# Kernel optimization log

Measured on AMD Instinct MI355X. Metric: run time of the kernel, lower is better.

## Reference

```python
import jax, jax.numpy as jnp
import numpy as np

N, D, E, L, H, F1, G, A = 4096, 256, 131072, 3, 4, 128, 16, 32

def setup_inputs() -> dict:
    key = jax.random.key(0)
    ks = jax.random.split(key, 12)
    s = lambda k, shape, fan: jax.random.normal(k, shape, jnp.float32) / np.sqrt(fan)
    return {
        "x": jax.random.normal(ks[0], (N, D), jnp.float32),
        "edge_attr": jax.random.uniform(ks[1], (E,), jnp.float32),
        "conv_Wself": s(ks[2], (L, D, D), D),
        "conv_Wnbr": s(ks[3], (L, D, D), D),
        "conv_b": jnp.zeros((L, D), jnp.float32),
        "bn_gamma": jnp.ones((L - 1, D), jnp.float32),
        "bn_beta": jnp.zeros((L - 1, D), jnp.float32),
        "bn_mean": jnp.zeros((L - 1, D), jnp.float32),
        "bn_var": jnp.ones((L - 1, D), jnp.float32),
        "Wqkv": s(ks[4], (3, D, D), D),
        "bqkv": jnp.zeros((3, D), jnp.float32),
        "Wo": s(ks[5], (D, D), D),
        "bo": jnp.zeros((D,), jnp.float32),
        "fc1_W": s(ks[6], (D, F1), D),
        "fc1_b": jnp.zeros((F1,), jnp.float32),
        "AW1": s(ks[7], (G, F1, A), F1),
        "Ab1": jnp.zeros((G, A), jnp.float32),
        "AW2": s(ks[8], (G, A, 1), A),
        "Ab2": jnp.zeros((G, 1), jnp.float32),
        "edge_index": jax.random.randint(ks[9], (2, E), 0, N, jnp.int32),
        "node_groups": jax.random.randint(ks[10], (N,), 0, G, jnp.int32),
    }


def reference(x, edge_attr, conv_Wself, conv_Wnbr, conv_b, bn_gamma, bn_beta,
              bn_mean, bn_var, Wqkv, bqkv, Wo, bo, fc1_W, fc1_b,
              AW1, Ab1, AW2, Ab2, edge_index, node_groups):
    src, dst = edge_index[0], edge_index[1]
    # message-passing conv stack (edge_attr only used by the last, non-attention layer)
    for i in range(L):
        msg = x[src]
        if i == L - 1:
            msg = msg * edge_attr[:, None]
        agg = jax.ops.segment_sum(msg, dst, num_segments=N)
        x = x @ conv_Wself[i] + agg @ conv_Wnbr[i] + conv_b[i]
        if i < L - 1:
            x = bn_gamma[i] * (x - bn_mean[i]) * jax.lax.rsqrt(bn_var[i] + 1e-5) + bn_beta[i]
            x = jax.nn.elu(x)
    # hierarchy self-attention over all N nodes (batch of 1), residual add
    dh = D // H
    q = (x @ Wqkv[0] + bqkv[0]).reshape(N, H, dh)
    k = (x @ Wqkv[1] + bqkv[1]).reshape(N, H, dh)
    v = (x @ Wqkv[2] + bqkv[2]).reshape(N, H, dh)
    scores = jnp.einsum('nhd,mhd->hnm', q, k) / np.sqrt(dh).astype(np.float32)
    attn = jax.nn.softmax(scores, axis=-1)
    o = jnp.einsum('hnm,mhd->nhd', attn, v).reshape(N, D) @ Wo + bo
    x = x + o
    feats = jax.nn.elu(x @ fc1_W + fc1_b)  # [N, F1]; dropout is eval no-op
    # MoE-style per-node group adapter routing: gather tiny MLP weights per node
    h = jax.nn.relu(jnp.einsum('nd,nda->na', feats, AW1[node_groups]) + Ab1[node_groups])
    out = jnp.einsum('na,nao->no', h, AW2[node_groups]) + Ab2[node_groups]  # [N, 1]
    return out
```

## Files before the change

### kernel.cpp

```cpp
#include <hip/hip_runtime.h>
#include <math.h>

#define NN   4096
#define DIM  256
#define NE   131072
#define NH   4
#define DH   64
#define F1D  128
#define NG   16
#define AD   32

typedef unsigned short u16;
typedef unsigned int   u32;
typedef _Float16 f16;
typedef __attribute__((ext_vector_type(8))) _Float16 half8;
typedef __attribute__((ext_vector_type(4))) float f32x4;

enum { EPI_BIAS = 0, EPI_BNELU = 1 };
enum { MEPI_WO = 0, MEPI_FC1 = 1 };

#define MFMA16(a, b, c) __builtin_amdgcn_mfma_f32_16x16x32_f16(a, b, c, 0, 0, 0)

__device__ inline u16 f2h(float x) { union { f16 f; u16 u; } c; c.f = (f16)x; return c.u; }
__device__ inline void split16(float x, u16& h, u16& l) {
    union { f16 f; u16 u; } ch, cl;
    ch.f = (f16)x;
    cl.f = (f16)(x - (float)ch.f);
    h = ch.u; l = cl.u;
}

__global__ void csr_count(const int* __restrict__ dst, int* __restrict__ cnt) {
    int e = blockIdx.x * 256 + threadIdx.x;
    atomicAdd(&cnt[dst[e]], 1);
}

__global__ __launch_bounds__(1024) void csr_scan(
    int* __restrict__ cnt, int* __restrict__ off)
{
    __shared__ int wsum[16];
    const int t = threadIdx.x;
    const int lane = t & 63;
    int4 v = *(const int4*)&cnt[t * 4];
    const int s = v.x + v.y + v.z + v.w;
    int acc = s;
    #pragma unroll
    for (int o = 1; o < 64; o <<= 1) {
        int u = __shfl_up(acc, o);
        if (lane >= o) acc += u;
    }
    if (lane == 63) wsum[t >> 6] = acc;
    __syncthreads();
    if (t < 16) {
        int w0 = wsum[t];
        int a2 = w0;
        #pragma unroll
        for (int o = 1; o < 16; o <<= 1) {
            int u = __shfl_up(a2, o);
            if (t >= o) a2 += u;
        }
        wsum[t] = a2 - w0;
    }
    __syncthreads();
    const int base = wsum[t >> 6] + (acc - s);
    off[t * 4 + 0] = base;
    off[t * 4 + 1] = base + v.x;
    off[t * 4 + 2] = base + v.x + v.y;
    off[t * 4 + 3] = base + v.x + v.y + v.z;
    *(int4*)&cnt[t * 4] = make_int4(0, 0, 0, 0);
    if (t == 1023) off[NN] = base + s;
}

__global__ void csr_fill(const int* __restrict__ dst, const int* __restrict__ src,
                         const float* __restrict__ eattr, const int* __restrict__ off,
                         int* __restrict__ cur, int* __restrict__ esrc,
                         float* __restrict__ ewt) {
    int e = blockIdx.x * 256 + threadIdx.x;
    int d = dst[e];
    int pos = off[d] + atomicAdd(&cur[d], 1);
    esrc[pos] = src[e];
    ewt[pos]  = eattr[e];
}

__global__ __launch_bounds__(256) void prep_kernel(
    const float* __restrict__ x,
    const float* __restrict__ Ws, const float* __restrict__ Wn,
    const float* __restrict__ Wqkv, const float* __restrict__ Wo,
    const float* __restrict__ fc1W,
    u16* __restrict__ xh, u16* __restrict__ xl,
    u16* __restrict__ wch, u16* __restrict__ wcl,
    u16* __restrict__ w4h, u16* __restrict__ w4l,
    u16* __restrict__ f1h, u16* __restrict__ f1l,
    int* __restrict__ cur)
{
    const int b = blockIdx.x;
    const int t = threadIdx.x;
    if (b < 1024) {
        const int gid = b * 256 + t;
        const float4 v = *(const float4*)&x[(size_t)gid * 4];
        u16 h[4], l[4];
        split16(v.x, h[0], l[0]); split16(v.y, h[1], l[1]);
        split16(v.z, h[2], l[2]); split16(v.w, h[3], l[3]);
        *(uint2*)&xh[(size_t)gid * 4] =
            make_uint2((u32)h[0] | ((u32)h[1] << 16), (u32)h[2] | ((u32)h[3] << 16));
        *(uint2*)&xl[(size_t)gid * 4] =
            make_uint2((u32)l[0] | ((u32)l[1] << 16), (u32)l[2] | ((u32)l[3] << 16));
    } else if (b < 1408) {
        const int gid = (b - 1024) * 256 + t;
        const int L = gid / 32768;
        const int rem = gid % 32768;
        const int m = rem / 128;
        const int k4 = (rem % 128) * 4;
        const float* S = Ws + (size_t)L * 65536;
        const float* Nb = Wn + (size_t)L * 65536;
        u16 h[4], l[4];
        #pragma unroll
        for (int j = 0; j < 4; ++j) {
            const int k = k4 + j;
            const float v = (k < 256) ? S[(size_t)k * 256 + m]
                                      : Nb[(size_t)(k - 256) * 256 + m];
            split16(v, h[j], l[j]);
        }
        const size_t o = (size_t)L * 131072 + (size_t)m * 512 + k4;
        *(uint2*)&wch[o] = make_uint2((u32)h[0] | ((u32)h[1] << 16), (u32)h[2] | ((u32)h[3] << 16));
        *(uint2*)&wcl[o] = make_uint2((u32)l[0] | ((u32)l[1] << 16), (u32)l[2] | ((u32)l[3] << 16));
    } else if (b < 1664) {
        const int gid = (b - 1408) * 256 + t;
        const int mat = gid / 16384;
        const int rem = gid % 16384;
        const int m = rem / 64;
        const int k4 = (rem % 64) * 4;
        const float* W = (mat < 3) ? Wqkv + (size_t)mat * 65536 : Wo;
        u16 h[4], l[4];
        #pragma unroll
        for (int j = 0; j < 4; ++j)
            split16(W[(size_t)(k4 + j) * 256 + m], h[j], l[j]);
        const size_t o = (size_t)mat * 65536 + (size_t)m * 256 + k4;
        *(uint2*)&w4h[o] = make_uint2((u32)h[0] | ((u32)h[1] << 16), (u32)h[2] | ((u32)h[3] << 16));
        *(uint2*)&w4l[o] = make_uint2((u32)l[0] | ((u32)l[1] << 16), (u32)l[2] | ((u32)l[3] << 16));
    } else if (b < 1696) {
        const int gid = (b - 1664) * 256 + t;
        const int m = gid / 64;
        const int k4 = (gid % 64) * 4;
        u16 h[4], l[4];
        #pragma unroll
        for (int j = 0; j < 4; ++j)
            split16(fc1W[(size_t)(k4 + j) * F1D + m], h[j], l[j]);
        const size_t o = (size_t)m * 256 + k4;
        *(uint2*)&f1h[o] = make_uint2((u32)h[0] | ((u32)h[1] << 16), (u32)h[2] | ((u32)h[3] << 16));
        *(uint2*)&f1l[o] = make_uint2((u32)l[0] | ((u32)l[1] << 16), (u32)l[2] | ((u32)l[3] << 16));
    } else {
        const int gid = (b - 1696) * 256 + t;
        if (gid < NN / 4) *(int4*)&cur[gid * 4] = make_int4(0, 0, 0, 0);
    }
}

template<bool LAST>
__global__ __launch_bounds__(256) void agg_kernel(
    const float* __restrict__ x, const int* __restrict__ esrc,
    const float* __restrict__ ewt, const int* __restrict__ off,
    u16* __restrict__ aggh, u16* __restrict__ aggl)
{
    const int node = blockIdx.x * 4 + (threadIdx.x >> 6);
    const int lane = threadIdx.x & 63;
    const int d4 = lane * 4;
    int j = off[node];
    const int j1 = off[node + 1];
    float4 acc = make_float4(0.f, 0.f, 0.f, 0.f);
    for (; j + 4 <= j1; j += 4) {
        const int s0 = esrc[j], s1 = esrc[j + 1], s2 = esrc[j + 2], s3 = esrc[j + 3];
        const float4 x0 = *(const float4*)&x[(size_t)s0 * DIM + d4];
        const float4 x1 = *(const float4*)&x[(size_t)s1 * DIM + d4];
        const float4 x2 = *(const float4*)&x[(size_t)s2 * DIM + d4];
        const float4 x3 = *(const float4*)&x[(size_t)s3 * DIM + d4];
        const float w0 = LAST ? ewt[j]     : 1.f;
        const float w1 = LAST ? ewt[j + 1] : 1.f;
        const float w2 = LAST ? ewt[j + 2] : 1.f;
        const float w3 = LAST ? ewt[j + 3] : 1.f;
        acc.x = fmaf(x0.x, w0, acc.x); acc.y = fmaf(x0.y, w0, acc.y);
        acc.z = fmaf(x0.z, w0, acc.z); acc.w = fmaf(x0.w, w0, acc.w);
        acc.x = fmaf(x1.x, w1, acc.x); acc.y = fmaf(x1.y, w1, acc.y);
        acc.z = fmaf(x1.z, w1, acc.z); acc.w = fmaf(x1.w, w1, acc.w);
        acc.x = fmaf(x2.x, w2, acc.x); acc.y = fmaf(x2.y, w2, acc.y);
        acc.z = fmaf(x2.z, w2, acc.z); acc.w = fmaf(x2.w, w2, acc.w);
        acc.x = fmaf(x3.x, w3, acc.x); acc.y = fmaf(x3.y, w3, acc.y);
        acc.z = fmaf(x3.z, w3, acc.z); acc.w = fmaf(x3.w, w3, acc.w);
    }
    for (; j < j1; ++j) {
        const int s = esrc[j];
        const float w = LAST ? ewt[j] : 1.f;
        const float4 xv = *(const float4*)&x[(size_t)s * DIM + d4];
        acc.x = fmaf(xv.x, w, acc.x); acc.y = fmaf(xv.y, w, acc.y);
        acc.z = fmaf(xv.z, w, acc.z); acc.w = fmaf(xv.w, w, acc.w);
    }
    u16 h[4], l[4];
    split16(acc.x, h[0], l[0]); split16(acc.y, h[1], l[1]);
    split16(acc.z, h[2], l[2]); split16(acc.w, h[3], l[3]);
    *(uint2*)&aggh[(size_t)node * DIM + d4] =
        make_uint2((u32)h[0] | ((u32)h[1] << 16), (u32)h[2] | ((u32)h[3] << 16));
    *(uint2*)&aggl[(size_t)node * DIM + d4] =
        make_uint2((u32)l[0] | ((u32)l[1] << 16), (u32)l[2] | ((u32)l[3] << 16));
}

template<int EPI>
__global__ __launch_bounds__(256) void conv_mfma(
    const u16* __restrict__ xh, const u16* __restrict__ xl,
    const u16* __restrict__ gh, const u16* __restrict__ gl,
    const u16* __restrict__ bth, const u16* __restrict__ btl,
    const float* __restrict__ bias,
    const float* __restrict__ gamma, const float* __restrict__ beta,
    const float* __restrict__ bnmean, const float* __restrict__ bnvar,
    float* __restrict__ outf, u16* __restrict__ oh, u16* __restrict__ ol)
{
    __shared__ u16 lds[13824];
    u16* As_h = lds;
    u16* As_l = lds + 2304;
    u16* Bs_h = lds + 4608;
    u16* Bs_l = lds + 9216;
    #define TKP 72

    const int tid  = threadIdx.x;
    const int row0 = blockIdx.y * 32;
    const int col0 = blockIdx.x * 64;

    const int w   = tid >> 6;
    const int l15 = tid & 15, h4 = (tid & 63) >> 4;
    const int rh  = w & 1, ch = w >> 1;
    const int arow = tid >> 3, acs = (tid & 7) * 8;
    const int brow = tid & 63, bseg = tid >> 6;
    const int bc = bseg * 16;

    uint4 sah, sal, sbh0, sbh1, sbl0, sbl1;
    {
        sah = *((const uint4*)&xh[(size_t)(row0 + arow) * DIM + acs]);
        sal = *((const uint4*)&xl[(size_t)(row0 + arow) * DIM + acs]);
        const u16* pbh = bth + (size_t)(col0 + brow) * 512 + bc;
        const u16* pbl = btl + (size_t)(col0 + brow) * 512 + bc;
        sbh0 = ((const uint4*)pbh)[0]; sbh1 = ((const uint4*)pbh)[1];
        sbl0 = ((const uint4*)pbl)[0]; sbl1 = ((const uint4*)pbl)[1];
    }

    const f32x4 z4 = {0.f, 0.f, 0.f, 0.f};
    f32x4 acc[2] = {z4, z4};

    for (int kt = 0; kt < 8; ++kt) {
        *(uint4*)&As_h[arow * TKP + acs] = sah;
        *(uint4*)&As_l[arow * TKP + acs] = sal;
        *(uint4*)&Bs_h[brow * TKP + bc]     = sbh0;
        *(uint4*)&Bs_h[brow * TKP + bc + 8] = sbh1;
        *(uint4*)&Bs_l[brow * TKP + bc]     = sbl0;
        *(uint4*)&Bs_l[brow * TKP + bc + 8] = sbl1;
        if (kt + 1 < 8) {
            const int kn = kt + 1;
            const u16 *pah, *pal;
            if (kn < 4) {
                pah = xh + (size_t)(row0 + arow) * DIM + kn * 64 + acs;
                pal = xl + (size_t)(row0 + arow) * DIM + kn * 64 + acs;
            } else {
                pah = gh + (size_t)(row0 + arow) * DIM + (kn - 4) * 64 + acs;
                pal = gl + (size_t)(row0 + arow) * DIM + (kn - 4) * 64 + acs;
            }
            sah = *((const uint4*)pah);
            sal = *((const uint4*)pal);
            const u16* pbh = bth + (size_t)(col0 + brow) * 512 + kn * 64 + bc;
            const u16* pbl = btl + (size_t)(col0 + brow) * 512 + kn * 64 + bc;
            sbh0 = ((const uint4*)pbh)[0]; sbh1 = ((const uint4*)pbh)[1];
            sbl0 = ((const uint4*)pbl)[0]; sbl1 = ((const uint4*)pbl)[1];
        }
        __syncthreads();

        __builtin_amdgcn_s_setprio(1);
        #pragma unroll
        for (int kc = 0; kc < 2; ++kc) {
            const int dc = kc * 32 + h4 * 8;
            half8 afh, afl, bfh[2], bfl[2];
            afh = *(const half8*)&As_h[(rh * 16 + l15) * TKP + dc];
            afl = *(const half8*)&As_l[(rh * 16 + l15) * TKP + dc];
            #pragma unroll
            for (int bb = 0; bb < 2; ++bb) {
                const int r = ch * 32 + bb * 16 + l15;
                bfh[bb] = *(const half8*)&Bs_h[r * TKP + dc];
                bfl[bb] = *(const half8*)&Bs_l[r * TKP + dc];
            }
            #pragma unroll
            for (int bb = 0; bb < 2; ++bb) {
                acc[bb] = MFMA16(afh, bfh[bb], acc[bb]);
                acc[bb] = MFMA16(afh, bfl[bb], acc[bb]);
                acc[bb] = MFMA16(afl, bfh[bb], acc[bb]);
            }
        }
        __builtin_amdgcn_s_setprio(0);
        __syncthreads();
    }

    #pragma unroll
    for (int bb = 0; bb < 2; ++bb) {
        const int c  = col0 + ch * 32 + bb * 16 + l15;
        const int r0 = row0 + rh * 16 + h4 * 4;
        #pragma unroll
        for (int i = 0; i < 4; ++i) {
            const int r = r0 + i;
            float t = acc[bb][i] + bias[c];
            if (EPI == EPI_BNELU) {
                t = gamma[c] * (t - bnmean[c]) * rsqrtf(bnvar[c] + 1e-5f) + beta[c];
                t = t > 0.f ? t : expm1f(t);
            }
            outf[(size_t)r * DIM + c] = t;
            u16 hh, ll;
            split16(t, hh, ll);
            oh[(size_t)r * DIM + c] = hh;
            ol[(size_t)r * DIM + c] = ll;
        }
    }
    #undef TKP
}

__global__ __launch_bounds__(256) void qkv_mfma(
    const u16* __restrict__ xh, const u16* __restrict__ xl,
    const u16* __restrict__ wth, const u16* __restrict__ wtl,
    const float* __restrict__ bias,
    u16* __restrict__ qh_o, u16* __restrict__ ql_o,
    u16* __restrict__ kh_o, u16* __restrict__ kl_o,
    u16* __restrict__ vt_o)
{
    __shared__ u16 lds[4 * 4608];
    u16* As_h = lds;
    u16* As_l = lds + 4608;
    u16* Bs_h = lds + 9216;
    u16* Bs_l = lds + 13824;
    #define TKP 72

    const int tid  = threadIdx.x;
    const int row0 = blockIdx.y * 64;
    const int mat  = blockIdx.x >> 2;
    const int col0 = (blockIdx.x & 3) * 64;
    const float* biasp = bias + mat * DIM;

    const int w   = tid >> 6;
    const int l15 = tid & 15, h4 = (tid & 63) >> 4;
    const int rh  = w & 1, ch = w >> 1;
    const int lrow = tid & 63, lseg = tid >> 6;
    const int lc = lseg * 16;

    const size_t brow = (size_t)(mat * 256 + col0 + lrow) * 256;
    uint4 sah0, sah1, sal0, sal1, sbh0, sbh1, sbl0, sbl1;
    {
        const u16* pah = xh + (size_t)(row0 + lrow) * DIM + lc;
        const u16* pal = xl + (size_t)(row0 + lrow) * DIM + lc;
        sah0 = ((const uint4*)pah)[0]; sah1 = ((const uint4*)pah)[1];
        sal0 = ((const uint4*)pal)[0]; sal1 = ((const uint4*)pal)[1];
        sbh0 = ((const uint4*)(wth + brow + lc))[0]; sbh1 = ((const uint4*)(wth + brow + lc))[1];
        sbl0 = ((const uint4*)(wtl + brow + lc))[0]; sbl1 = ((const uint4*)(wtl + brow + lc))[1];
    }

    const f32x4 z4 = {0.f, 0.f, 0.f, 0.f};
    f32x4 acc[2][2] = {{z4, z4}, {z4, z4}};

    for (int kt = 0; kt < 4; ++kt) {
        *(uint4*)&As_h[lrow * TKP + lc]     = sah0;
        *(uint4*)&As_h[lrow * TKP + lc + 8] = sah1;
        *(uint4*)&As_l[lrow * TKP + lc]     = sal0;
        *(uint4*)&As_l[lrow * TKP + lc + 8] = sal1;
        *(uint4*)&Bs_h[lrow * TKP + lc]     = sbh0;
        *(uint4*)&Bs_h[lrow * TKP + lc + 8] = sbh1;
        *(uint4*)&Bs_l[lrow * TKP + lc]     = sbl0;
        *(uint4*)&Bs_l[lrow * TKP + lc + 8] = sbl1;
        if (kt + 1 < 4) {
            const int kb = (kt + 1) * 64 + lc;
            const u16* pah = xh + (size_t)(row0 + lrow) * DIM + kb;
            const u16* pal = xl + (size_t)(row0 + lrow) * DIM + kb;
            sah0 = ((const uint4*)pah)[0]; sah1 = ((const uint4*)pah)[1];
            sal0 = ((const uint4*)pal)[0]; sal1 = ((const uint4*)pal)[1];
            sbh0 = ((const uint4*)(wth + brow + kb))[0]; sbh1 = ((const uint4*)(wth + brow + kb))[1];
            sbl0 = ((const uint4*)(wtl + brow + kb))[0]; sbl1 = ((const uint4*)(wtl + brow + kb))[1];
        }
        __syncthreads();

        __builtin_amdgcn_s_setprio(1);
        #pragma unroll
        for (int kc = 0; kc < 2; ++kc) {
            const int dc = kc * 32 + h4 * 8;
            half8 afh[2], afl[2], bfh[2], bfl[2];
            #pragma unroll
            for (int ab = 0; ab < 2; ++ab) {
                const int r = rh * 32 + ab * 16 + l15;
                afh[ab] = *(const half8*)&As_h[r * TKP + dc];
                afl[ab] = *(const half8*)&As_l[r * TKP + dc];
            }
            #pragma unroll
            for (int bb = 0; bb < 2; ++bb) {
                const int r = ch * 32 + bb * 16 + l15;
                bfh[bb] = *(const half8*)&Bs_h[r * TKP + dc];
                bfl[bb] = *(const half8*)&Bs_l[r * TKP + dc];
            }
            #pragma unroll
            for (int ab = 0; ab < 2; ++ab)
                #pragma unroll
                for (int bb = 0; bb < 2; ++bb) {
                    acc[ab][bb] = MFMA16(afh[ab], bfh[bb], acc[ab][bb]);
                    acc[ab][bb] = MFMA16(afh[ab], bfl[bb], acc[ab][bb]);
                    acc[ab][bb] = MFMA16(afl[ab], bfh[bb], acc[ab][bb]);
                }
        }
        __builtin_amdgcn_s_setprio(0);
        __syncthreads();
    }

    const float s = (mat == 0) ? 0.125f : 1.0f;
    u16* oph = (mat == 0) ? qh_o : kh_o;
    u16* opl = (mat == 0) ? ql_o : kl_o;
    #pragma unroll
    for (int ab = 0; ab < 2; ++ab)
        #pragma unroll
        for (int bb = 0; bb < 2; ++bb) {
            const int c  = col0 + ch * 32 + bb * 16 + l15;
            const int r0 = row0 + rh * 32 + ab * 16 + h4 * 4;
            if (mat < 2) {
                #pragma unroll
                for (int i = 0; i < 4; ++i) {
                    const int r = r0 + i;
                    const float t = (acc[ab][bb][i] + biasp[c]) * s;
                    u16 hh, ll;
                    split16(t, hh, ll);
                    oph[(size_t)r * DIM + c] = hh;
                    opl[(size_t)r * DIM + c] = ll;
                }
            } else {
                u16 v[4];
                #pragma unroll
                for (int i = 0; i < 4; ++i)
                    v[i] = f2h(acc[ab][bb][i] + biasp[c]);
                *(uint2*)&vt_o[(size_t)c * NN + r0] =
                    make_uint2((u32)v[0] | ((u32)v[1] << 16), (u32)v[2] | ((u32)v[3] << 16));
            }
        }
    #undef TKP
}

template<int MEPI>
__global__ __launch_bounds__(256) void mfma_gemm(
    const u16* __restrict__ Ah, const u16* __restrict__ Al,
    const u16* __restrict__ Bth, const u16* __restrict__ Btl,
    const float* __restrict__ bias, const float* __restrict__ resid,
    float* __restrict__ outf, u16* __restrict__ outh, u16* __restrict__ outl,
    int K, int M)
{
    __shared__ u16 lds[4 * 4608];
    u16* As_h = lds;
    u16* As_l = lds + 4608;
    u16* Bs_h = lds + 9216;
    u16* Bs_l = lds + 13824;
    #define TKP 72

    const int tid  = threadIdx.x;
    const int row0 = blockIdx.y * 64;
    const int col0 = blockIdx.x * 64;

    const int w   = tid >> 6;
    const int l15 = tid & 15, h4 = (tid & 63) >> 4;
    const int rh  = w & 1, ch = w >> 1;
    const int lrow = tid & 63, lseg = tid >> 6;
    const int lc = lseg * 16;

    uint4 sah0, sah1, sal0, sal1, sbh0, sbh1, sbl0, sbl1;
    {
        const u16* pa0 = Ah  + (size_t)(row0 + lrow) * K + lc;
        const u16* pa1 = Al  + (size_t)(row0 + lrow) * K + lc;
        const u16* pb0 = Bth + (size_t)(col0 + lrow) * K + lc;
        const u16* pb1 = Btl + (size_t)(col0 + lrow) * K + lc;
        sah0 = ((const uint4*)pa0)[0]; sah1 = ((const uint4*)pa0)[1];
        sal0 = ((const uint4*)pa1)[0]; sal1 = ((const uint4*)pa1)[1];
        sbh0 = ((const uint4*)pb0)[0]; sbh1 = ((const uint4*)pb0)[1];
        sbl0 = ((const uint4*)pb1)[0]; sbl1 = ((const uint4*)pb1)[1];
    }

    const f32x4 z4 = {0.f, 0.f, 0.f, 0.f};
    f32x4 acc[2][2] = {{z4, z4}, {z4, z4}};
    const int NKT2 = K / 64;

    for (int kt = 0; kt < NKT2; ++kt) {
        *(uint4*)&As_h[lrow * TKP + lc]     = sah0;
        *(uint4*)&As_h[lrow * TKP + lc + 8] = sah1;
        *(uint4*)&As_l[lrow * TKP + lc]     = sal0;
        *(uint4*)&As_l[lrow * TKP + lc + 8] = sal1;
        *(uint4*)&Bs_h[lrow * TKP + lc]     = sbh0;
        *(uint4*)&Bs_h[lrow * TKP + lc + 8] = sbh1;
        *(uint4*)&Bs_l[lrow * TKP + lc]     = sbl0;
        *(uint4*)&Bs_l[lrow * TKP + lc + 8] = sbl1;
        if (kt + 1 < NKT2) {
            const int kb = (kt + 1) * 64 + lc;
            const u16* pa0 = Ah  + (size_t)(row0 + lrow) * K + kb;
            const u16* pa1 = Al  + (size_t)(row0 + lrow) * K + kb;
            const u16* pb0 = Bth + (size_t)(col0 + lrow) * K + kb;
            const u16* pb1 = Btl + (size_t)(col0 + lrow) * K + kb;
            sah0 = ((const uint4*)pa0)[0]; sah1 = ((const uint4*)pa0)[1];
            sal0 = ((const uint4*)pa1)[0]; sal1 = ((const uint4*)pa1)[1];
            sbh0 = ((const uint4*)pb0)[0]; sbh1 = ((const uint4*)pb0)[1];
            sbl0 = ((const uint4*)pb1)[0]; sbl1 = ((const uint4*)pb1)[1];
        }
        __syncthreads();

        __builtin_amdgcn_s_setprio(1);
        #pragma unroll
        for (int kc = 0; kc < 2; ++kc) {
            const int dc = kc * 32 + h4 * 8;
            half8 afh[2], afl[2], bfh[2], bfl[2];
            #pragma unroll
            for (int ab = 0; ab < 2; ++ab) {
                const int r = rh * 32 + ab * 16 + l15;
                afh[ab] = *(const half8*)&As_h[r * TKP + dc];
                afl[ab] = *(const half8*)&As_l[r * TKP + dc];
            }
            #pragma unroll
            for (int bb = 0; bb < 2; ++bb) {
                const int r = ch * 32 + bb * 16 + l15;
                bfh[bb] = *(const half8*)&Bs_h[r * TKP + dc];
                bfl[bb] = *(const half8*)&Bs_l[r * TKP + dc];
            }
            #pragma unroll
            for (int ab = 0; ab < 2; ++ab)
                #pragma unroll
                for (int bb = 0; bb < 2; ++bb) {
                    acc[ab][bb] = MFMA16(afh[ab], bfh[bb], acc[ab][bb]);
                    acc[ab][bb] = MFMA16(afh[ab], bfl[bb], acc[ab][bb]);
                    acc[ab][bb] = MFMA16(afl[ab], bfh[bb], acc[ab][bb]);
                }
        }
        __builtin_amdgcn_s_setprio(0);
        __syncthreads();
    }

    #pragma unroll
    for (int ab = 0; ab < 2; ++ab)
        #pragma unroll
        for (int bb = 0; bb < 2; ++bb) {
            const int c  = col0 + ch * 32 + bb * 16 + l15;
            const int r0 = row0 + rh * 32 + ab * 16 + h4 * 4;
            #pragma unroll
            for (int i = 0; i < 4; ++i) {
                const int r = r0 + i;
                float t = acc[ab][bb][i] + bias[c];
                if (MEPI == MEPI_WO) {
                    t += resid[(size_t)r * M + c];
                    u16 hh, ll;
                    split16(t, hh, ll);
                    outh[(size_t)r * M + c] = hh;
                    outl[(size_t)r * M + c] = ll;
                } else {
                    t = t > 0.f ? t : expm1f(t);
                    outf[(size_t)r * M + c] = t;
                }
            }
        }
    #undef TKP
}

#define QB 64
#define KB 64
#define NSPLIT 4
#define NKT (NN / KB)
#define KP 72

__global__ __launch_bounds__(256, 2) void attn_kernel(
    const u16* __restrict__ qhi, const u16* __restrict__ qlo,
    const u16* __restrict__ khi, const u16* __restrict__ klo,
    const u16* __restrict__ vT,
    float* __restrict__ op0, float* __restrict__ op1,
    float* __restrict__ op2, float* __restrict__ op3,
    float* __restrict__ mpart, float* __restrict__ lpart)
{
    __shared__ u16 lds[32384];
    u16* Kh0 = lds;
    u16* Kl0 = lds + 4608;
    u16* Vt0 = lds + 9216;
    u16* Kh1 = lds + 13824;
    u16* Kl1 = lds + 18432;
    u16* Vt1 = lds + 23040;
    u16* Pb  = lds + 27648;
    u16* Qh  = lds;
    u16* Ql  = lds + 4608;
    float* frow = (float*)(lds + 32256);

    const int tid = threadIdx.x;
    const int h   = blockIdx.y;
    const int q0  = blockIdx.x * QB;
    const int sp  = blockIdx.z;
    const int kt0 = sp * (NKT / NSPLIT);
    const int kt1 = kt0 + NKT / NSPLIT;

    const int w   = tid >> 6;
    const int l15 = tid & 15, h4 = (tid & 63) >> 4;
    const int lrow = tid & 63, lseg = tid >> 6;
    const int gq = h * DH + lseg * 16;

    {
        const u16* s0 = qhi + (size_t)(q0 + lrow) * DIM + gq;
        const u16* s1 = qlo + (size_t)(q0 + lrow) * DIM + gq;
        uint4 a = ((const uint4*)s0)[0], b = ((const uint4*)s0)[1];
        uint4 c = ((const uint4*)s1)[0], d = ((const uint4*)s1)[1];
        *(uint4*)&Qh[lrow * KP + lseg * 16]     = a;
        *(uint4*)&Qh[lrow * KP + lseg * 16 + 8] = b;
        *(uint4*)&Ql[lrow * KP + lseg * 16]     = c;
        *(uint4*)&Ql[lrow * KP + lseg * 16 + 8] = d;
    }

    uint4 rk0, rk1, rl0, rl1, rv0, rv1;
    auto load_tile = [&](int kt_ld) {
        const int key0 = kt_ld * KB;
        const u16* s0 = khi + (size_t)(key0 + lrow) * DIM + gq;
        const u16* s1 = klo + (size_t)(key0 + lrow) * DIM + gq;
        const u16* s2 = vT + (size_t)(h * DH + lrow) * NN + key0 + lseg * 16;
        rk0 = ((const uint4*)s0)[0]; rk1 = ((const uint4*)s0)[1];
        rl0 = ((const uint4*)s1)[0]; rl1 = ((const uint4*)s1)[1];
        rv0 = ((const uint4*)s2)[0]; rv1 = ((const uint4*)s2)[1];
    };
    load_tile(kt0);
    __syncthreads();

    half8 qf[2][2];
    #pragma unroll
    for (int kc = 0; kc < 2; ++kc) {
        const int r = w * 16 + l15;
        const int dc = kc * 32 + h4 * 8;
        qf[kc][0] = *(const half8*)&Qh[r * KP + dc];
        qf[kc][1] = *(const half8*)&Ql[r * KP + dc];
    }
    __syncthreads();

    auto stage_to = [&](u16* Kh, u16* Kl, u16* Vt) {
        *(uint4*)&Kh[lrow * KP + lseg * 16]     = rk0;
        *(uint4*)&Kh[lrow * KP + lseg * 16 + 8] = rk1;
        *(uint4*)&Kl[lrow * KP + lseg * 16]     = rl0;
        *(uint4*)&Kl[lrow * KP + lseg * 16 + 8] = rl1;
        *(uint4*)&Vt[lrow * KP + lseg * 16]     = rv0;
        *(uint4*)&Vt[lrow * KP + lseg * 16 + 8] = rv1;
    };

    stage_to(Kh0, Kl0, Vt0);
    load_tile(kt0 + 1);
    __syncthreads();

    const f32x4 z4 = {0.f, 0.f, 0.f, 0.f};
    f32x4 oacc[4] = {z4, z4, z4, z4};
    float m_run[4], l_run[4];
    #pragma unroll
    for (int i = 0; i < 4; ++i) { m_run[i] = -3.0e38f; l_run[i] = 0.f; }

    auto tile_body = [&](int t, u16* Kc, u16* Lc, u16* Vc,
                         u16* Kn, u16* Ln, u16* Vn) {
        if (t + 1 < kt1) stage_to(Kn, Ln, Vn);
        if (t + 2 < kt1) load_tile(t + 2);

        f32x4 sc[4] = {z4, z4, z4, z4};
        __builtin_amdgcn_s_setprio(1);
        #pragma unroll
        for (int kc = 0; kc < 2; ++kc) {
            const int dc = kc * 32 + h4 * 8;
            half8 kfh[4], kfl[4];
            #pragma unroll
            for (int kcb = 0; kcb < 4; ++kcb) {
                const int r = kcb * 16 + l15;
                kfh[kcb] = *(const half8*)&Kc[r * KP + dc];
                kfl[kcb] = *(const half8*)&Lc[r * KP + dc];
            }
            #pragma unroll
            for (int kcb = 0; kcb < 4; ++kcb) {
                sc[kcb] = MFMA16(qf[kc][0], kfh[kcb], sc[kcb]);
                sc[kcb] = MFMA16(qf[kc][0], kfl[kcb], sc[kcb]);
                sc[kcb] = MFMA16(qf[kc][1], kfh[kcb], sc[kcb]);
            }
        }
        __builtin_amdgcn_s_setprio(0);
        float p[4][4], fr[4];
        #pragma unroll
        for (int i = 0; i < 4; ++i) {
            float pm = fmaxf(fmaxf(sc[0][i], sc[1][i]), fmaxf(sc[2][i], sc[3][i]));
            #pragma unroll
            for (int off = 1; off < 16; off <<= 1)
                pm = fmaxf(pm, __shfl_xor(pm, off));
            const float mnew = fmaxf(m_run[i], pm);
            fr[i] = __expf(m_run[i] - mnew);
            m_run[i] = mnew;
            p[0][i] = __expf(sc[0][i] - mnew);
            p[1][i] = __expf(sc[1][i] - mnew);
            p[2][i] = __expf(sc[2][i] - mnew);
            p[3][i] = __expf(sc[3][i] - mnew);
            float ls = (p[0][i] + p[1][i]) + (p[2][i] + p[3][i]);
            #pragma unroll
            for (int off = 1; off < 16; off <<= 1) ls += __shfl_xor(ls, off);
            l_run[i] = l_run[i] * fr[i] + ls;
        }
        #pragma unroll
        for (int kcb = 0; kcb < 4; ++kcb) {
            const int kk = kcb * 16 + l15;
            #pragma unroll
            for (int i = 0; i < 4; ++i)
                Pb[(w * 16 + h4 * 4 + i) * KP + kk] = f2h(p[kcb][i]);
        }
        if (l15 == 0) {
            #pragma unroll
            for (int i = 0; i < 4; ++i)
                frow[w * 16 + h4 * 4 + i] = fr[i];
        }
        const float frq = frow[w * 16 + l15];
        #pragma unroll
        for (int db = 0; db < 4; ++db) oacc[db] *= frq;
        __builtin_amdgcn_s_setprio(1);
        #pragma unroll
        for (int kc = 0; kc < 2; ++kc) {
            const half8 pf = *(const half8*)&Pb[(w * 16 + l15) * KP + kc * 32 + h4 * 8];
            #pragma unroll
            for (int db = 0; db < 4; ++db) {
                const half8 vf = *(const half8*)&Vc[(db * 16 + l15) * KP + kc * 32 + h4 * 8];
                oacc[db] = MFMA16(vf, pf, oacc[db]);
            }
        }
        __builtin_amdgcn_s_setprio(0);
        __syncthreads();
    };

    for (int t = kt0; t < kt1; t += 2) {
        tile_body(t,     Kh0, Kl0, Vt0, Kh1, Kl1, Vt1);
        tile_body(t + 1, Kh1, Kl1, Vt1, Kh0, Kl0, Vt0);
    }

    float* ob = (sp == 0) ? op0 : ((sp == 1) ? op1 : ((sp == 2) ? op2 : op3));
    #pragma unroll
    for (int db = 0; db < 4; ++db)
        *(f32x4*)&ob[(size_t)(q0 + w * 16 + l15) * DIM + h * DH + db * 16 + h4 * 4] = oacc[db];
    if (l15 == 0) {
        #pragma unroll
        for (int i = 0; i < 4; ++i) {
            const int r = w * 16 + h4 * 4 + i;
            mpart[((size_t)sp * NN + q0 + r) * NH + h] = m_run[i];
            lpart[((size_t)sp * NN + q0 + r) * NH + h] = l_run[i];
        }
    }
}

__global__ __launch_bounds__(256) void attn_combine(
    const float* __restrict__ o0, const float* __restrict__ o1,
    const float* __restrict__ o2, const float* __restrict__ o3,
    const float* __restrict__ mp, const float* __restrict__ lp,
    u16* __restrict__ ohi, u16* __restrict__ olo)
{
    const int gid = blockIdx.x * 256 + threadIdx.x;
    const int row = gid >> 6;
    const int c4  = (gid & 63) * 4;
    const int h   = c4 >> 6;
    float m[4], wgt[4];
    #pragma unroll
    for (int z = 0; z < 4; ++z) m[z] = mp[((size_t)z * NN + row) * NH + h];
    const float M = fmaxf(fmaxf(m[0], m[1]), fmaxf(m[2], m[3]));
    float den = 0.f;
    #pragma unroll
    for (int z = 0; z < 4; ++z) {
        wgt[z] = __expf(m[z] - M);
        den += lp[((size_t)z * NN + row) * NH + h] * wgt[z];
    }
    const float inv = 1.f / den;
    const float4 a = *(const float4*)&o0[(size_t)row * DIM + c4];
    const float4 b = *(const float4*)&o1[(size_t)row * DIM + c4];
    const float4 c = *(const float4*)&o2[(size_t)row * DIM + c4];
    const float4 d = *(const float4*)&o3[(size_t)row * DIM + c4];
    float r[4];
    r[0] = (a.x * wgt[0] + b.x * wgt[1] + c.x * wgt[2] + d.x * wgt[3]) * inv;
    r[1] = (a.y * wgt[0] + b.y * wgt[1] + c.y * wgt[2] + d.y * wgt[3]) * inv;
    r[2] = (a.z * wgt[0] + b.z * wgt[1] + c.z * wgt[2] + d.z * wgt[3]) * inv;
    r[3] = (a.w * wgt[0] + b.w * wgt[1] + c.w * wgt[2] + d.w * wgt[3]) * inv;
    u16 hh[4], ll[4];
    #pragma unroll
    for (int j = 0; j < 4; ++j) split16(r[j], hh[j], ll[j]);
    *(uint2*)&ohi[(size_t)row * DIM + c4] =
        make_uint2((u32)hh[0] | ((u32)hh[1] << 16), (u32)hh[2] | ((u32)hh[3] << 16));
    *(uint2*)&olo[(size_t)row * DIM + c4] =
        make_uint2((u32)ll[0] | ((u32)ll[1] << 16), (u32)ll[2] | ((u32)ll[3] << 16));
}

__global__ __launch_bounds__(64) void adapter_kernel(
    const float* __restrict__ feats, const int* __restrict__ grp,
    const float* __restrict__ AW1, const float* __restrict__ Ab1,
    const float* __restrict__ AW2, const float* __restrict__ Ab2,
    float* __restrict__ out)
{
    const int n = blockIdx.x;
    const int lane = threadIdx.x;
    __shared__ float f[F1D];
    f[lane]      = feats[(size_t)n * F1D + lane];
    f[lane + 64] = feats[(size_t)n * F1D + 64 + lane];
    __syncthreads();
    const int g = grp[n];
    const float* W1 = AW1 + (size_t)g * F1D * AD;
    const int a = lane & 31;
    const int half = lane >> 5;
    float hsum = 0.f;
    for (int d = 0; d < 64; ++d)
        hsum = fmaf(f[half * 64 + d], W1[(half * 64 + d) * AD + a], hsum);
    hsum += __shfl_xor(hsum, 32);
    hsum = fmaxf(hsum + Ab1[g * AD + a], 0.f);
    float p = hsum * AW2[g * AD + a];
    #pragma unroll
    for (int mm = 1; mm < 32; mm <<= 1) p += __shfl_xor(p, mm);
    if (lane == 0) out[n] = p + Ab2[g];
}

extern "C" void kernel_launch(void* const* d_in, const int* in_sizes, int n_in,
                              void* d_out, int out_size, void* d_ws, size_t ws_size,
                              hipStream_t stream)
{
    const float* x_in   = (const float*)d_in[0];
    const float* eattr  = (const float*)d_in[1];
    const float* Wself  = (const float*)d_in[2];
    const float* Wnbr   = (const float*)d_in[3];
    const float* convb  = (const float*)d_in[4];
    const float* gamma  = (const float*)d_in[5];
    const float* beta   = (const float*)d_in[6];
    const float* bnmean = (const float*)d_in[7];
    const float* bnvar  = (const float*)d_in[8];
    const float* Wqkv   = (const float*)d_in[9];
    const float* bqkv   = (const float*)d_in[10];
    const float* Wo     = (const float*)d_in[11];
    const float* bo     = (const float*)d_in[12];
    const float* fc1W   = (const float*)d_in[13];
    const float* fc1b   = (const float*)d_in[14];
    const float* AW1    = (const float*)d_in[15];
    const float* Ab1    = (const float*)d_in[16];
    const float* AW2    = (const float*)d_in[17];
    const float* Ab2    = (const float*)d_in[18];
    const int*   eidx   = (const int*)d_in[19];
    const int*   grp    = (const int*)d_in[20];
    const int* srcArr = eidx;
    const int* dstArr = eidx + NE;

    float* fws = (float*)d_ws;
    const size_t NM = (size_t)NN * DIM;
    float* bufA  = fws;
    float* bufB  = fws + NM;
    float* bufC  = fws + 2 * NM;
    float* feats = fws + 3 * NM;
    float* mpart = fws + 3 * NM + NM / 2;
    float* lpart = mpart + 4 * NN * NH;
    u16* up = (u16*)(lpart + 4 * NN * NH);
    u16* xpAh = up;             u16* xpAl = xpAh + NM;
    u16* xpBh = xpAl + NM;      u16* xpBl = xpBh + NM;
    u16* aggh = xpBl + NM;      u16* aggl = aggh + NM;
    u16* qh = aggl + NM;        u16* ql = qh + NM;
    u16* kh = ql + NM;          u16* kl = kh + NM;
    u16* vt = kl + NM;
    u16* wcath = vt + NM;
    u16* wcatl = wcath + 3 * 131072;
    u16* wt4h  = wcatl + 3 * 131072;
    u16* wt4l  = wt4h + 4 * 65536;
    u16* fc1h  = wt4l + 4 * 65536;
    u16* fc1l  = fc1h + 32768;
    int*   esrc = (int*)(fc1l + 32768);
    float* ewt  = (float*)(esrc + NE);
    int* off    = (int*)(ewt + NE);
    int* cur    = off + NN + 1;
    float* outp = (float*)d_out;

    float* op2 = (float*)xpAh;
    float* op3 = (float*)xpBh;

    prep_kernel<<<1700, 256, 0, stream>>>(
        x_in, Wself, Wnbr, Wqkv, Wo, fc1W,
        xpAh, xpAl, wcath, wcatl, wt4h, wt4l, fc1h, fc1l, cur);

    csr_count<<<NE / 256, 256, 0, stream>>>(dstArr, cur);
    csr_scan<<<1, 1024, 0, stream>>>(cur, off);
    csr_fill<<<NE / 256, 256, 0, stream>>>(dstArr, srcArr, eattr, off, cur, esrc, ewt);

    const dim3 gc(DIM / 64, NN / 32);
    const int rgrid = NN * DIM / 4 / 256;

    agg_kernel<false><<<NN / 4, 256, 0, stream>>>(x_in, esrc, ewt, off, aggh, aggl);
    conv_mfma<EPI_BNELU><<<gc, 256, 0, stream>>>(
        xpAh, xpAl, aggh, aggl, wcath, wcatl, convb,
        gamma, beta, bnmean, bnvar, bufA, xpBh, xpBl);
    agg_kernel<false><<<NN / 4, 256, 0, stream>>>(bufA, esrc, ewt, off, aggh, aggl);
    conv_mfma<EPI_BNELU><<<gc, 256, 0, stream>>>(
        xpBh, xpBl, aggh, aggl, wcath + 131072, wcatl + 131072, convb + DIM,
        gamma + DIM, beta + DIM, bnmean + DIM, bnvar + DIM, bufC, xpAh, xpAl);
    agg_kernel<true><<<NN / 4, 256, 0, stream>>>(bufC, esrc, ewt, off, aggh, aggl);
    conv_mfma<EPI_BIAS><<<gc, 256, 0, stream>>>(
        xpAh, xpAl, aggh, aggl, wcath + 262144, wcatl + 262144, convb + 2 * DIM,
        nullptr, nullptr, nullptr, nullptr, bufA, xpBh, xpBl);

    qkv_mfma<<<dim3(12, NN / 64), 256, 0, stream>>>(
        xpBh, xpBl, wt4h, wt4l, bqkv, qh, ql, kh, kl, vt);

    attn_kernel<<<dim3(NN / QB, NH, NSPLIT), 256, 0, stream>>>(
        qh, ql, kh, kl, vt, bufB, bufC, op2, op3, mpart, lpart);
    attn_combine<<<rgrid, 256, 0, stream>>>(
        bufB, bufC, op2, op3, mpart, lpart, qh, ql);

    mfma_gemm<MEPI_WO><<<dim3(DIM / 64, NN / 64), 256, 0, stream>>>(
        qh, ql, wt4h + 3 * 65536, wt4l + 3 * 65536, bo, bufA,
        nullptr, kh, kl, DIM, DIM);

    mfma_gemm<MEPI_FC1><<<dim3(F1D / 64, NN / 64), 256, 0, stream>>>(
        kh, kl, fc1h, fc1l, fc1b, nullptr, feats, nullptr, nullptr, DIM, F1D);

    adapter_kernel<<<NN, 64, 0, stream>>>(feats, grp, AW1, Ab1, AW2, Ab2, outp);
}
```

Measured before the change: 243.1 us.

## Double attention query tile to 128 rows with 512-thread blocks

The attention kernel now handles 128 query rows per block with 8 waves instead of 64 rows with 4 waves. Each staged K/V tile in LDS is therefore reused by twice as many queries, roughly halving global K/V traffic and staging work per query. Per-thread load and stage work shrinks to one uint4 per buffer, and the LDS layout grows to fit the larger Q and P regions. In exchange the grid has half as many blocks and each block uses more LDS, which can cut occupancy and latency hiding.

```diff
diff --git a/kernel.cpp b/kernel.cpp
--- a/kernel.cpp
+++ b/kernel.cpp
@@ -554,13 +554,13 @@
     #undef TKP
 }
 
-#define QB 64
+#define QB 128
 #define KB 64
 #define NSPLIT 4
 #define NKT (NN / KB)
 #define KP 72
 
-__global__ __launch_bounds__(256, 2) void attn_kernel(
+__global__ __launch_bounds__(512, 2) void attn_kernel(
     const u16* __restrict__ qhi, const u16* __restrict__ qlo,
     const u16* __restrict__ khi, const u16* __restrict__ klo,
     const u16* __restrict__ vT,
@@ -568,7 +568,7 @@
     float* __restrict__ op2, float* __restrict__ op3,
     float* __restrict__ mpart, float* __restrict__ lpart)
 {
-    __shared__ u16 lds[32384];
+    __shared__ u16 lds[37120];
     u16* Kh0 = lds;
     u16* Kl0 = lds + 4608;
     u16* Vt0 = lds + 9216;
@@ -577,8 +577,8 @@
     u16* Vt1 = lds + 23040;
     u16* Pb  = lds + 27648;
     u16* Qh  = lds;
-    u16* Ql  = lds + 4608;
-    float* frow = (float*)(lds + 32256);
+    u16* Ql  = lds + 13824;
+    float* frow = (float*)(lds + 36864);
 
     const int tid = threadIdx.x;
     const int h   = blockIdx.y;
@@ -590,28 +590,26 @@
     const int w   = tid >> 6;
     const int l15 = tid & 15, h4 = (tid & 63) >> 4;
     const int lrow = tid & 63, lseg = tid >> 6;
-    const int gq = h * DH + lseg * 16;
+    const int gq8 = h * DH + lseg * 8;
 
     {
-        const u16* s0 = qhi + (size_t)(q0 + lrow) * DIM + gq;
-        const u16* s1 = qlo + (size_t)(q0 + lrow) * DIM + gq;
+        const int qrow = tid >> 2, qseg = tid & 3;
+        const u16* s0 = qhi + (size_t)(q0 + qrow) * DIM + h * DH + qseg * 16;
+        const u16* s1 = qlo + (size_t)(q0 + qrow) * DIM + h * DH + qseg * 16;
         uint4 a = ((const uint4*)s0)[0], b = ((const uint4*)s0)[1];
         uint4 c = ((const uint4*)s1)[0], d = ((const uint4*)s1)[1];
-        *(uint4*)&Qh[lrow * KP + lseg * 16]     = a;
-        *(uint4*)&Qh[lrow * KP + lseg * 16 + 8] = b;
-        *(uint4*)&Ql[lrow * KP + lseg * 16]     = c;
-        *(uint4*)&Ql[lrow * KP + lseg * 16 + 8] = d;
-    }
-
-    uint4 rk0, rk1, rl0, rl1, rv0, rv1;
+        *(uint4*)&Qh[qrow * KP + qseg * 16]     = a;
+        *(uint4*)&Qh[qrow * KP + qseg * 16 + 8] = b;
+        *(uint4*)&Ql[qrow * KP + qseg * 16]     = c;
+        *(uint4*)&Ql[qrow * KP + qseg * 16 + 8] = d;
+    }
+
+    uint4 rk, rl, rv;
     auto load_tile = [&](int kt_ld) {
         const int key0 = kt_ld * KB;
-        const u16* s0 = khi + (size_t)(key0 + lrow) * DIM + gq;
-        const u16* s1 = klo + (size_t)(key0 + lrow) * DIM + gq;
-        const u16* s2 = vT + (size_t)(h * DH + lrow) * NN + key0 + lseg * 16;
-        rk0 = ((const uint4*)s0)[0]; rk1 = ((const uint4*)s0)[1];
-        rl0 = ((const uint4*)s1)[0]; rl1 = ((const uint4*)s1)[1];
-        rv0 = ((const uint4*)s2)[0]; rv1 = ((const uint4*)s2)[1];
+        rk = *(const uint4*)(khi + (size_t)(key0 + lrow) * DIM + gq8);
+        rl = *(const uint4*)(klo + (size_t)(key0 + lrow) * DIM + gq8);
+        rv = *(const uint4*)(vT + (size_t)(h * DH + lrow) * NN + key0 + lseg * 8);
     };
     load_tile(kt0);
     __syncthreads();
@@ -627,12 +625,9 @@
     __syncthreads();
 
     auto stage_to = [&](u16* Kh, u16* Kl, u16* Vt) {
-        *(uint4*)&Kh[lrow * KP + lseg * 16]     = rk0;
-        *(uint4*)&Kh[lrow * KP + lseg * 16 + 8] = rk1;
-        *(uint4*)&Kl[lrow * KP + lseg * 16]     = rl0;
-        *(uint4*)&Kl[lrow * KP + lseg * 16 + 8] = rl1;
-        *(uint4*)&Vt[lrow * KP + lseg * 16]     = rv0;
-        *(uint4*)&Vt[lrow * KP + lseg * 16 + 8] = rv1;
+        *(uint4*)&Kh[lrow * KP + lseg * 8] = rk;
+        *(uint4*)&Kl[lrow * KP + lseg * 8] = rl;
+        *(uint4*)&Vt[lrow * KP + lseg * 8] = rv;
     };
 
     stage_to(Kh0, Kl0, Vt0);
@@ -888,7 +883,7 @@
     qkv_mfma<<<dim3(12, NN / 64), 256, 0, stream>>>(
         xpBh, xpBl, wt4h, wt4l, bqkv, qh, ql, kh, kl, vt);
 
-    attn_kernel<<<dim3(NN / QB, NH, NSPLIT), 256, 0, stream>>>(
+    attn_kernel<<<dim3(NN / QB, NH, NSPLIT), 512, 0, stream>>>(
         qh, ql, kh, kl, vt, bufB, bufC, op2, op3, mpart, lpart);
     attn_combine<<<rgrid, 256, 0, stream>>>(
         bufB, bufC, op2, op3, mpart, lpart, qh, ql);
```

Result: faster. 237.1 us (-2.5%).
